# Kernel tuning notes

Measured on AMD Instinct MI355X. Metric: run time of the kernel, lower is better.

## Reference

```python
import jax, jax.numpy as jnp
import numpy as np

B, N, C, HEADS = 4, 8192, 512, 8


def setup_inputs() -> dict:
    key = jax.random.key(0)
    k1, k2, k3, k4, k5 = jax.random.split(key, 5)
    s = 1.0 / np.sqrt(C)
    return {
        "x": jax.random.normal(k1, (B, N, C), dtype=jnp.float32),
        "w_qkv": jax.random.normal(k2, (3 * C, C), dtype=jnp.float32) * s,
        "b_qkv": jax.random.normal(k3, (3 * C,), dtype=jnp.float32) * 0.01,
        "w_fc": jax.random.normal(k4, (C, C), dtype=jnp.float32) * s,
        "b_fc": jax.random.normal(k5, (C,), dtype=jnp.float32) * 0.01,
        "heads": HEADS,
    }


def reference(x, w_qkv, b_qkv, w_fc, b_fc, heads):
    b, n, c = x.shape
    d = c // heads
    scale = d ** (-0.5)
    # torch Linear: y = x @ W.T + b
    qkv = (x @ w_qkv.T + b_qkv).reshape(b, n, 3, heads, d)
    q, k, v = qkv[:, :, 0], qkv[:, :, 1], qkv[:, :, 2]  # [b,n,h,d]
    # NOTE: source does NOT move heads to dim 1, so attention is over the
    # heads axis: dots is [b, n, h, h].
    dots = jnp.einsum("bnhd,bngd->bnhg", q, k) * scale
    dots = jnp.clip(dots, -50.0, 50.0)
    attn = jax.nn.softmax(dots, axis=-1)
    out = jnp.einsum("bnhg,bngd->bnhd", attn, v)  # [b,n,h,d]
    # transpose(1,2).reshape(B,N,C) exactly as in torch (scrambles n/h)
    out = out.transpose(0, 2, 1, 3).reshape(b, n, c)
    return out @ w_fc.T + b_fc
```

## Files before the change

### kernel.cpp

```cpp
#include <hip/hip_runtime.h>
#include <hip/hip_bf16.h>
#include <stdint.h>


typedef __bf16 bf16x8 __attribute__((ext_vector_type(8)));
typedef float f32x4 __attribute__((ext_vector_type(4)));

__device__ __forceinline__ unsigned short f2bf(float f) {
  unsigned u = __float_as_uint(f);
  u += 0x7fffu + ((u >> 16) & 1u);
  return (unsigned short)(u >> 16);
}
__device__ __forceinline__ unsigned pk2(float a, float b) {
  return (unsigned)f2bf(a) | ((unsigned)f2bf(b) << 16);
}
__device__ __forceinline__ void unpk2(unsigned u, float& a, float& b) {
  a = __uint_as_float(u << 16);
  b = __uint_as_float(u & 0xffff0000u);
}
__device__ __forceinline__ void gload_lds16(const void* g, void* l) {
  __builtin_amdgcn_global_load_lds((const __attribute__((address_space(1))) void*)g,
                                   (__attribute__((address_space(3))) void*)l,
                                   16, 0, 0);
}

__global__ __launch_bounds__(256) void cvt_f32_to_bf16(const float* __restrict__ in,
                                                       __hip_bfloat16* __restrict__ out,
                                                       int n8) {
  int i = blockIdx.x * 256 + threadIdx.x;
  if (i >= n8) return;
  const float4* p = (const float4*)in;
  float4 a = p[i * 2];
  float4 b = p[i * 2 + 1];
  uint4 o;
  o.x = pk2(a.x, a.y);
  o.y = pk2(a.z, a.w);
  o.z = pk2(b.x, b.y);
  o.w = pk2(b.z, b.w);
  ((uint4*)out)[i] = o;
}


#define STG(S, BUF)                                                                       \
  do {                                                                                    \
    int _k0 = (S) * 32;                                                                   \
    gload_lds16(Ag + (size_t)(bm0 + srowA0) * KDIM + _k0 + skofA0,                        \
                lds + (BUF) * 24576 + dstA0);                                             \
    gload_lds16(Ag + (size_t)(bm0 + srowA1) * KDIM + _k0 + skofA1,                        \
                lds + (BUF) * 24576 + dstA1);                                             \
    gload_lds16(Bg + (size_t)(bn0 + srowB) * KDIM + _k0 + skofB,                          \
                lds + (BUF) * 24576 + 16384 + dstB);                                      \
  } while (0)

template <bool OUT_BF16, int KDIM>
__global__ __launch_bounds__(512, 4) void gemm3b(const __hip_bfloat16* __restrict__ Ag,
                                                 const __hip_bfloat16* __restrict__ Bg,
                                                 const float* __restrict__ bias,
                                                 void* __restrict__ C,
                                                 int M, int N, int NT) {
  __shared__ __align__(16) char lds[73728];

  const int tid = threadIdx.x;
  const int wv = tid >> 6;
  const int ln = tid & 63;
  const int lrow = ln & 15;
  const int kg = ln >> 4;
  const int wm = wv >> 1;
  const int wn = wv & 1;

  int nwg = gridDim.x;
  int cpx = nwg >> 3;
  int bs = (blockIdx.x & 7) * cpx + (blockIdx.x >> 3);
  const int bm0 = (bs / NT) * 256;
  const int bn0 = (bs % NT) * 128;

  const int pbase = (lrow >> 1) * 128 + ((((lrow & 1) << 2) | kg) ^ ((lrow >> 1) & 7)) * 16;

  int srowA0, skofA0, dstA0, srowA1, skofA1, dstA1, srowB, skofB, dstB;
  {
    int L0 = wv * 1024 + ln * 16;
    int rp0 = L0 >> 7, T0 = ((L0 >> 4) & 7) ^ (rp0 & 7);
    srowA0 = rp0 * 2 + (T0 >> 2);
    skofA0 = (T0 & 3) * 8;
    dstA0 = wv * 1024;
    int L1 = 8192 + L0;
    int rp1 = L1 >> 7, T1 = ((L1 >> 4) & 7) ^ (rp1 & 7);
    srowA1 = rp1 * 2 + (T1 >> 2);
    skofA1 = (T1 & 3) * 8;
    dstA1 = 8192 + wv * 1024;
    srowB = srowA0;
    skofB = skofA0;
    dstB = wv * 1024;
  }

  f32x4 acc[4][4] = {};

  constexpr int NKT = KDIM >> 5;

  STG(0, 0);
  STG(1, 1);

#pragma unroll
  for (int s = 0; s < NKT; ++s) {
    if (s == NKT - 1) {
      asm volatile("s_waitcnt vmcnt(0)" ::: "memory");
    } else {
      asm volatile("s_waitcnt vmcnt(3)" ::: "memory");
    }
    __builtin_amdgcn_s_barrier();
    __builtin_amdgcn_sched_barrier(0);
    if (s + 2 < NKT) STG(s + 2, (s + 2) % 3);
    {
      const char* _ab = lds + (s % 3) * 24576 + wm * 4096 + pbase;
      const char* _bb = lds + (s % 3) * 24576 + 16384 + wn * 4096 + pbase;
      bf16x8 a0 = *(const bf16x8*)(_ab);
      bf16x8 a1 = *(const bf16x8*)(_ab + 1024);
      bf16x8 a2 = *(const bf16x8*)(_ab + 2048);
      bf16x8 a3 = *(const bf16x8*)(_ab + 3072);
      bf16x8 b0 = *(const bf16x8*)(_bb);
      bf16x8 b1 = *(const bf16x8*)(_bb + 1024);
      bf16x8 b2 = *(const bf16x8*)(_bb + 2048);
      bf16x8 b3 = *(const bf16x8*)(_bb + 3072);
      asm volatile("s_waitcnt lgkmcnt(0)" ::: "memory");
      __builtin_amdgcn_sched_barrier(0);
      __builtin_amdgcn_s_setprio(1);
      acc[0][0] = __builtin_amdgcn_mfma_f32_16x16x32_bf16(a0, b0, acc[0][0], 0, 0, 0);
      acc[0][1] = __builtin_amdgcn_mfma_f32_16x16x32_bf16(a0, b1, acc[0][1], 0, 0, 0);
      acc[0][2] = __builtin_amdgcn_mfma_f32_16x16x32_bf16(a0, b2, acc[0][2], 0, 0, 0);
      acc[0][3] = __builtin_amdgcn_mfma_f32_16x16x32_bf16(a0, b3, acc[0][3], 0, 0, 0);
      acc[1][0] = __builtin_amdgcn_mfma_f32_16x16x32_bf16(a1, b0, acc[1][0], 0, 0, 0);
      acc[1][1] = __builtin_amdgcn_mfma_f32_16x16x32_bf16(a1, b1, acc[1][1], 0, 0, 0);
      acc[1][2] = __builtin_amdgcn_mfma_f32_16x16x32_bf16(a1, b2, acc[1][2], 0, 0, 0);
      acc[1][3] = __builtin_amdgcn_mfma_f32_16x16x32_bf16(a1, b3, acc[1][3], 0, 0, 0);
      acc[2][0] = __builtin_amdgcn_mfma_f32_16x16x32_bf16(a2, b0, acc[2][0], 0, 0, 0);
      acc[2][1] = __builtin_amdgcn_mfma_f32_16x16x32_bf16(a2, b1, acc[2][1], 0, 0, 0);
      acc[2][2] = __builtin_amdgcn_mfma_f32_16x16x32_bf16(a2, b2, acc[2][2], 0, 0, 0);
      acc[2][3] = __builtin_amdgcn_mfma_f32_16x16x32_bf16(a2, b3, acc[2][3], 0, 0, 0);
      acc[3][0] = __builtin_amdgcn_mfma_f32_16x16x32_bf16(a3, b0, acc[3][0], 0, 0, 0);
      acc[3][1] = __builtin_amdgcn_mfma_f32_16x16x32_bf16(a3, b1, acc[3][1], 0, 0, 0);
      acc[3][2] = __builtin_amdgcn_mfma_f32_16x16x32_bf16(a3, b2, acc[3][2], 0, 0, 0);
      acc[3][3] = __builtin_amdgcn_mfma_f32_16x16x32_bf16(a3, b3, acc[3][3], 0, 0, 0);
      __builtin_amdgcn_s_setprio(0);
    }
  }
  __syncthreads();

  if (OUT_BF16) {
    unsigned short* tile = (unsigned short*)lds;
#pragma unroll
    for (int fi = 0; fi < 4; ++fi) {
#pragma unroll
      for (int cj = 0; cj < 4; ++cj) {
        int col = wn * 64 + cj * 16 + lrow;
        float bv = bias[bn0 + col];
#pragma unroll
        for (int r = 0; r < 4; ++r) {
          int row = wm * 64 + fi * 16 + kg * 4 + r;
          int sc = (((col >> 3) ^ (row & 7)) << 3) | (col & 7);
          tile[row * 128 + sc] = f2bf(acc[fi][cj][r] + bv);
        }
      }
    }
    __syncthreads();
#pragma unroll
    for (int it = 0; it < 8; ++it) {
      int id = it * 512 + tid;
      int row = id >> 4;
      int c = id & 15;
      uint4 v = *(const uint4*)(lds + row * 256 + ((c ^ (row & 7)) << 4));
      *(uint4*)((unsigned short*)C + (size_t)(bm0 + row) * N + bn0 + c * 8) = v;
    }
  } else {
    float* tilef = (float*)lds;
#pragma unroll
    for (int pass = 0; pass < 2; ++pass) {
      if ((wm >> 1) == pass) {
#pragma unroll
        for (int fi = 0; fi < 4; ++fi) {
#pragma unroll
          for (int cj = 0; cj < 4; ++cj) {
            int col = wn * 64 + cj * 16 + lrow;
            float bv = bias[bn0 + col];
#pragma unroll
            for (int r = 0; r < 4; ++r) {
              int row = (wm & 1) * 64 + fi * 16 + kg * 4 + r;
              int sc = (((col >> 2) ^ (row & 7)) << 2) | (col & 3);
              tilef[row * 128 + sc] = acc[fi][cj][r] + bv;
            }
          }
        }
      }
      __syncthreads();
#pragma unroll
      for (int it = 0; it < 8; ++it) {
        int id = it * 512 + tid;
        int row = id >> 5;
        int c = id & 31;
        uint4 v = *(const uint4*)(lds + row * 512 + ((c ^ (row & 7)) << 4));
        *(uint4*)((float*)C + (size_t)(bm0 + pass * 128 + row) * N + bn0 + c * 4) = v;
      }
      __syncthreads();
    }
  }
}

__global__ __launch_bounds__(256) void attn_tok(const __hip_bfloat16* __restrict__ qkv,
                                                __hip_bfloat16* __restrict__ outp,
                                                int ntok, int npb) {
  const int wv = threadIdx.x >> 6;
  const int ln = threadIdx.x & 63;
  const int t = blockIdx.x * 4 + wv;
  if (t >= ntok) return;
  const int m = ln & 7;

  const __hip_bfloat16* row = qkv + (size_t)t * 1536;
  uint4 qr = *(const uint4*)(row + ln * 8);
  uint4 kr = *(const uint4*)(row + 512 + ln * 8);
  uint4 vr = *(const uint4*)(row + 1024 + ln * 8);

  float qf[8];
  unpk2(qr.x, qf[0], qf[1]);
  unpk2(qr.y, qf[2], qf[3]);
  unpk2(qr.z, qf[4], qf[5]);
  unpk2(qr.w, qf[6], qf[7]);
  unsigned kw[4] = {kr.x, kr.y, kr.z, kr.w};
  unsigned vw[4] = {vr.x, vr.y, vr.z, vr.w};

  float dt[8];
#pragma unroll
  for (int g = 0; g < 8; ++g) {
    int src = g * 8 + m;
    float s = 0.f;
#pragma unroll
    for (int j4 = 0; j4 < 4; ++j4) {
      unsigned kk = __shfl(kw[j4], src, 64);
      float a, b;
      unpk2(kk, a, b);
      s += qf[j4 * 2] * a + qf[j4 * 2 + 1] * b;
    }
    s += __shfl_xor(s, 1, 64);
    s += __shfl_xor(s, 2, 64);
    s += __shfl_xor(s, 4, 64);
    dt[g] = s;
  }

  float mx = -1e30f;
#pragma unroll
  for (int g = 0; g < 8; ++g) {
    dt[g] = fminf(fmaxf(dt[g] * 0.125f, -50.f), 50.f);
    mx = fmaxf(mx, dt[g]);
  }
  float p[8], ssum = 0.f;
#pragma unroll
  for (int g = 0; g < 8; ++g) {
    p[g] = __expf(dt[g] - mx);
    ssum += p[g];
  }
  float inv = 1.f / ssum;

  float o[8] = {0, 0, 0, 0, 0, 0, 0, 0};
#pragma unroll
  for (int g = 0; g < 8; ++g) {
    int src = g * 8 + m;
    float ag = p[g] * inv;
#pragma unroll
    for (int j4 = 0; j4 < 4; ++j4) {
      unsigned vv = __shfl(vw[j4], src, 64);
      float a, b;
      unpk2(vv, a, b);
      o[j4 * 2] += ag * a;
      o[j4 * 2 + 1] += ag * b;
    }
  }

  const int h = ln >> 3;
  const int b = t / npb, n = t % npb;
  size_t dst = (size_t)b * npb * 512 + (size_t)(h * (npb >> 3) + (n >> 3)) * 512 +
               (size_t)((n & 7) * 64 + m * 8);
  uint4 ov;
  ov.x = pk2(o[0], o[1]);
  ov.y = pk2(o[2], o[3]);
  ov.z = pk2(o[4], o[5]);
  ov.w = pk2(o[6], o[7]);
  *(uint4*)(outp + dst) = ov;
}

extern "C" void kernel_launch(void* const* d_in, const int* in_sizes, int n_in,
                              void* d_out, int out_size, void* d_ws, size_t ws_size,
                              hipStream_t stream) {
  const float* x = (const float*)d_in[0];
  const float* w_qkv = (const float*)d_in[1];
  const float* b_qkv = (const float*)d_in[2];
  const float* w_fc = (const float*)d_in[3];
  const float* b_fc = (const float*)d_in[4];
  float* out = (float*)d_out;

  const int M = 32768;
  const int Cc = 512, N3 = 1536;

  __hip_bfloat16* xb = (__hip_bfloat16*)d_ws;
  __hip_bfloat16* wqkvb = xb + (size_t)M * Cc;
  __hip_bfloat16* wfcb = wqkvb + (size_t)N3 * Cc;
  __hip_bfloat16* qkvb = wfcb + (size_t)Cc * Cc;
  __hip_bfloat16* attb = qkvb + (size_t)M * N3;

  cvt_f32_to_bf16<<<(M * Cc / 8) / 256, 256, 0, stream>>>(x, xb, M * Cc / 8);
  cvt_f32_to_bf16<<<(N3 * Cc / 8) / 256, 256, 0, stream>>>(w_qkv, wqkvb, N3 * Cc / 8);
  cvt_f32_to_bf16<<<(Cc * Cc / 8) / 256, 256, 0, stream>>>(w_fc, wfcb, Cc * Cc / 8);

  gemm3b<true, 512><<<(M / 256) * (N3 / 128), 512, 0, stream>>>(xb, wqkvb, b_qkv, qkvb, M, N3,
                                                                N3 / 128);
  attn_tok<<<M / 4, 256, 0, stream>>>(qkvb, attb, M, 8192);
  gemm3b<false, 512><<<(M / 256) * (Cc / 128), 512, 0, stream>>>(attb, wfcb, b_fc, out, M, Cc,
                                                                 Cc / 128);
}
```

Measured before the change: 147.4 us.

## Use 4-wave GEMM blocks with 128x64 per-wave tiles

Restructures the GEMM kernel from 8 waves of 64x64 subtiles to 4 waves of 128x64 subtiles over the same 256x128 block tile. Each wave now issues 6 global-to-LDS loads per stage and keeps 32 accumulators, which raises the MFMA-to-LDS-read ratio and halves barrier participants. The cost is higher register pressure and fewer waves to hide latency, and the launch bounds change to 256 threads with 2 blocks per unit.

```diff
diff --git a/kernel.cpp b/kernel.cpp
--- a/kernel.cpp
+++ b/kernel.cpp
@@ -44,16 +44,18 @@
 #define STG(S, BUF)                                                                       \
   do {                                                                                    \
     int _k0 = (S) * 32;                                                                   \
-    gload_lds16(Ag + (size_t)(bm0 + srowA0) * KDIM + _k0 + skofA0,                        \
-                lds + (BUF) * 24576 + dstA0);                                             \
-    gload_lds16(Ag + (size_t)(bm0 + srowA1) * KDIM + _k0 + skofA1,                        \
-                lds + (BUF) * 24576 + dstA1);                                             \
-    gload_lds16(Bg + (size_t)(bn0 + srowB) * KDIM + _k0 + skofB,                          \
-                lds + (BUF) * 24576 + 16384 + dstB);                                      \
+    _Pragma("unroll") for (int _j = 0; _j < 4; ++_j) {                                    \
+      gload_lds16(Ag + (size_t)(bm0 + srowA[_j]) * KDIM + _k0 + skofA[_j],                \
+                  lds + (BUF) * 24576 + _j * 4096 + wv * 1024);                           \
+    }                                                                                     \
+    _Pragma("unroll") for (int _j = 0; _j < 2; ++_j) {                                    \
+      gload_lds16(Bg + (size_t)(bn0 + srowB[_j]) * KDIM + _k0 + skofB[_j],                \
+                  lds + (BUF) * 24576 + 16384 + _j * 4096 + wv * 1024);                   \
+    }                                                                                     \
   } while (0)
 
 template <bool OUT_BF16, int KDIM>
-__global__ __launch_bounds__(512, 4) void gemm3b(const __hip_bfloat16* __restrict__ Ag,
+__global__ __launch_bounds__(256, 2) void gemm4w(const __hip_bfloat16* __restrict__ Ag,
                                                  const __hip_bfloat16* __restrict__ Bg,
                                                  const float* __restrict__ bias,
                                                  void* __restrict__ C,
@@ -76,24 +78,20 @@
 
   const int pbase = (lrow >> 1) * 128 + ((((lrow & 1) << 2) | kg) ^ ((lrow >> 1) & 7)) * 16;
 
-  int srowA0, skofA0, dstA0, srowA1, skofA1, dstA1, srowB, skofB, dstB;
-  {
-    int L0 = wv * 1024 + ln * 16;
-    int rp0 = L0 >> 7, T0 = ((L0 >> 4) & 7) ^ (rp0 & 7);
-    srowA0 = rp0 * 2 + (T0 >> 2);
-    skofA0 = (T0 & 3) * 8;
-    dstA0 = wv * 1024;
-    int L1 = 8192 + L0;
-    int rp1 = L1 >> 7, T1 = ((L1 >> 4) & 7) ^ (rp1 & 7);
-    srowA1 = rp1 * 2 + (T1 >> 2);
-    skofA1 = (T1 & 3) * 8;
-    dstA1 = 8192 + wv * 1024;
-    srowB = srowA0;
-    skofB = skofA0;
-    dstB = wv * 1024;
-  }
-
-  f32x4 acc[4][4] = {};
+  int srowA[4], skofA[4], srowB[2], skofB[2];
+#pragma unroll
+  for (int j = 0; j < 4; ++j) {
+    int L = j * 4096 + wv * 1024 + ln * 16;
+    int rp = L >> 7, T = ((L >> 4) & 7) ^ (rp & 7);
+    srowA[j] = rp * 2 + (T >> 2);
+    skofA[j] = (T & 3) * 8;
+    if (j < 2) {
+      srowB[j] = srowA[j];
+      skofB[j] = skofA[j];
+    }
+  }
+
+  f32x4 acc[8][4] = {};
 
   constexpr int NKT = KDIM >> 5;
 
@@ -105,41 +103,29 @@
     if (s == NKT - 1) {
       asm volatile("s_waitcnt vmcnt(0)" ::: "memory");
     } else {
-      asm volatile("s_waitcnt vmcnt(3)" ::: "memory");
+      asm volatile("s_waitcnt vmcnt(6)" ::: "memory");
     }
     __builtin_amdgcn_s_barrier();
     __builtin_amdgcn_sched_barrier(0);
     if (s + 2 < NKT) STG(s + 2, (s + 2) % 3);
     {
-      const char* _ab = lds + (s % 3) * 24576 + wm * 4096 + pbase;
+      const char* _ab = lds + (s % 3) * 24576 + wm * 8192 + pbase;
       const char* _bb = lds + (s % 3) * 24576 + 16384 + wn * 4096 + pbase;
-      bf16x8 a0 = *(const bf16x8*)(_ab);
-      bf16x8 a1 = *(const bf16x8*)(_ab + 1024);
-      bf16x8 a2 = *(const bf16x8*)(_ab + 2048);
-      bf16x8 a3 = *(const bf16x8*)(_ab + 3072);
-      bf16x8 b0 = *(const bf16x8*)(_bb);
-      bf16x8 b1 = *(const bf16x8*)(_bb + 1024);
-      bf16x8 b2 = *(const bf16x8*)(_bb + 2048);
-      bf16x8 b3 = *(const bf16x8*)(_bb + 3072);
+      bf16x8 af[8];
+      bf16x8 bf[4];
+#pragma unroll
+      for (int fi = 0; fi < 8; ++fi) af[fi] = *(const bf16x8*)(_ab + fi * 1024);
+#pragma unroll
+      for (int cj = 0; cj < 4; ++cj) bf[cj] = *(const bf16x8*)(_bb + cj * 1024);
       asm volatile("s_waitcnt lgkmcnt(0)" ::: "memory");
       __builtin_amdgcn_sched_barrier(0);
       __builtin_amdgcn_s_setprio(1);
-      acc[0][0] = __builtin_amdgcn_mfma_f32_16x16x32_bf16(a0, b0, acc[0][0], 0, 0, 0);
-      acc[0][1] = __builtin_amdgcn_mfma_f32_16x16x32_bf16(a0, b1, acc[0][1], 0, 0, 0);
-      acc[0][2] = __builtin_amdgcn_mfma_f32_16x16x32_bf16(a0, b2, acc[0][2], 0, 0, 0);
-      acc[0][3] = __builtin_amdgcn_mfma_f32_16x16x32_bf16(a0, b3, acc[0][3], 0, 0, 0);
-      acc[1][0] = __builtin_amdgcn_mfma_f32_16x16x32_bf16(a1, b0, acc[1][0], 0, 0, 0);
-      acc[1][1] = __builtin_amdgcn_mfma_f32_16x16x32_bf16(a1, b1, acc[1][1], 0, 0, 0);
-      acc[1][2] = __builtin_amdgcn_mfma_f32_16x16x32_bf16(a1, b2, acc[1][2], 0, 0, 0);
-      acc[1][3] = __builtin_amdgcn_mfma_f32_16x16x32_bf16(a1, b3, acc[1][3], 0, 0, 0);
-      acc[2][0] = __builtin_amdgcn_mfma_f32_16x16x32_bf16(a2, b0, acc[2][0], 0, 0, 0);
-      acc[2][1] = __builtin_amdgcn_mfma_f32_16x16x32_bf16(a2, b1, acc[2][1], 0, 0, 0);
-      acc[2][2] = __builtin_amdgcn_mfma_f32_16x16x32_bf16(a2, b2, acc[2][2], 0, 0, 0);
-      acc[2][3] = __builtin_amdgcn_mfma_f32_16x16x32_bf16(a2, b3, acc[2][3], 0, 0, 0);
-      acc[3][0] = __builtin_amdgcn_mfma_f32_16x16x32_bf16(a3, b0, acc[3][0], 0, 0, 0);
-      acc[3][1] = __builtin_amdgcn_mfma_f32_16x16x32_bf16(a3, b1, acc[3][1], 0, 0, 0);
-      acc[3][2] = __builtin_amdgcn_mfma_f32_16x16x32_bf16(a3, b2, acc[3][2], 0, 0, 0);
-      acc[3][3] = __builtin_amdgcn_mfma_f32_16x16x32_bf16(a3, b3, acc[3][3], 0, 0, 0);
+#pragma unroll
+      for (int fi = 0; fi < 8; ++fi)
+#pragma unroll
+        for (int cj = 0; cj < 4; ++cj)
+          acc[fi][cj] =
+              __builtin_amdgcn_mfma_f32_16x16x32_bf16(af[fi], bf[cj], acc[fi][cj], 0, 0, 0);
       __builtin_amdgcn_s_setprio(0);
     }
   }
@@ -148,14 +134,14 @@
   if (OUT_BF16) {
     unsigned short* tile = (unsigned short*)lds;
 #pragma unroll
-    for (int fi = 0; fi < 4; ++fi) {
+    for (int fi = 0; fi < 8; ++fi) {
 #pragma unroll
       for (int cj = 0; cj < 4; ++cj) {
         int col = wn * 64 + cj * 16 + lrow;
         float bv = bias[bn0 + col];
 #pragma unroll
         for (int r = 0; r < 4; ++r) {
-          int row = wm * 64 + fi * 16 + kg * 4 + r;
+          int row = wm * 128 + fi * 16 + kg * 4 + r;
           int sc = (((col >> 3) ^ (row & 7)) << 3) | (col & 7);
           tile[row * 128 + sc] = f2bf(acc[fi][cj][r] + bv);
         }
@@ -163,8 +149,8 @@
     }
     __syncthreads();
 #pragma unroll
-    for (int it = 0; it < 8; ++it) {
-      int id = it * 512 + tid;
+    for (int it = 0; it < 16; ++it) {
+      int id = it * 256 + tid;
       int row = id >> 4;
       int c = id & 15;
       uint4 v = *(const uint4*)(lds + row * 256 + ((c ^ (row & 7)) << 4));
@@ -174,16 +160,16 @@
     float* tilef = (float*)lds;
 #pragma unroll
     for (int pass = 0; pass < 2; ++pass) {
-      if ((wm >> 1) == pass) {
-#pragma unroll
-        for (int fi = 0; fi < 4; ++fi) {
+      if (wm == pass) {
+#pragma unroll
+        for (int fi = 0; fi < 8; ++fi) {
 #pragma unroll
           for (int cj = 0; cj < 4; ++cj) {
             int col = wn * 64 + cj * 16 + lrow;
             float bv = bias[bn0 + col];
 #pragma unroll
             for (int r = 0; r < 4; ++r) {
-              int row = (wm & 1) * 64 + fi * 16 + kg * 4 + r;
+              int row = fi * 16 + kg * 4 + r;
               int sc = (((col >> 2) ^ (row & 7)) << 2) | (col & 3);
               tilef[row * 128 + sc] = acc[fi][cj][r] + bv;
             }
@@ -192,8 +178,8 @@
       }
       __syncthreads();
 #pragma unroll
-      for (int it = 0; it < 8; ++it) {
-        int id = it * 512 + tid;
+      for (int it = 0; it < 16; ++it) {
+        int id = it * 256 + tid;
         int row = id >> 5;
         int c = id & 31;
         uint4 v = *(const uint4*)(lds + row * 512 + ((c ^ (row & 7)) << 4));
@@ -308,9 +294,9 @@
   cvt_f32_to_bf16<<<(N3 * Cc / 8) / 256, 256, 0, stream>>>(w_qkv, wqkvb, N3 * Cc / 8);
   cvt_f32_to_bf16<<<(Cc * Cc / 8) / 256, 256, 0, stream>>>(w_fc, wfcb, Cc * Cc / 8);
 
-  gemm3b<true, 512><<<(M / 256) * (N3 / 128), 512, 0, stream>>>(xb, wqkvb, b_qkv, qkvb, M, N3,
+  gemm4w<true, 512><<<(M / 256) * (N3 / 128), 256, 0, stream>>>(xb, wqkvb, b_qkv, qkvb, M, N3,
                                                                 N3 / 128);
   attn_tok<<<M / 4, 256, 0, stream>>>(qkvb, attb, M, 8192);
-  gemm3b<false, 512><<<(M / 256) * (Cc / 128), 512, 0, stream>>>(attb, wfcb, b_fc, out, M, Cc,
+  gemm4w<false, 512><<<(M / 256) * (Cc / 128), 256, 0, stream>>>(attb, wfcb, b_fc, out, M, Cc,
                                                                  Cc / 128);
 }
```

New measurement: 154.5 us. +4.9%, slower.

## Switch GEMM to 32x32x16 MFMA tiles and fuse the three conversion kernels

Applied to the files above, without the earlier changes.

The GEMM inner loop moves from sixteen 16x16x32 MFMAs per k-step to eight 32x32x16 MFMAs on four 32x32 accumulators. LDS fragment addressing and the epilogue row/column mapping change to match the 32x32 output layout. The aim is fewer MFMA issues and fewer LDS reads per unit of work. The three f32-to-bf16 conversion launches are also merged into a single kernel that picks its source by index range, which removes two launch overheads. The risk is that the new lane-to-element mapping, which relies on the swizzle, gives wrong results if it does not line up with the staging layout.

```diff
diff --git a/kernel.cpp b/kernel.cpp
--- a/kernel.cpp
+++ b/kernel.cpp
@@ -5,6 +5,7 @@
 
 typedef __bf16 bf16x8 __attribute__((ext_vector_type(8)));
 typedef float f32x4 __attribute__((ext_vector_type(4)));
+typedef float f32x16 __attribute__((ext_vector_type(16)));
 
 __device__ __forceinline__ unsigned short f2bf(float f) {
   unsigned u = __float_as_uint(f);
@@ -24,20 +25,34 @@
                                    16, 0, 0);
 }
 
-__global__ __launch_bounds__(256) void cvt_f32_to_bf16(const float* __restrict__ in,
-                                                       __hip_bfloat16* __restrict__ out,
-                                                       int n8) {
+__global__ __launch_bounds__(256) void cvt_all(const float* __restrict__ x,
+                                               const float* __restrict__ wq,
+                                               const float* __restrict__ wf,
+                                               unsigned short* __restrict__ xb,
+                                               unsigned short* __restrict__ wqb,
+                                               unsigned short* __restrict__ wfb) {
+  const int n0 = 2097152;
+  const int n1 = 98304;
   int i = blockIdx.x * 256 + threadIdx.x;
-  if (i >= n8) return;
+  const float* in;
+  unsigned short* ob;
+  int j;
+  if (i < n0) {
+    in = x; ob = xb; j = i;
+  } else if (i < n0 + n1) {
+    in = wq; ob = wqb; j = i - n0;
+  } else {
+    in = wf; ob = wfb; j = i - n0 - n1;
+  }
   const float4* p = (const float4*)in;
-  float4 a = p[i * 2];
-  float4 b = p[i * 2 + 1];
+  float4 a = p[j * 2];
+  float4 b = p[j * 2 + 1];
   uint4 o;
   o.x = pk2(a.x, a.y);
   o.y = pk2(a.z, a.w);
   o.z = pk2(b.x, b.y);
   o.w = pk2(b.z, b.w);
-  ((uint4*)out)[i] = o;
+  ((uint4*)ob)[j] = o;
 }
 
 
@@ -53,7 +68,7 @@
   } while (0)
 
 template <bool OUT_BF16, int KDIM>
-__global__ __launch_bounds__(512, 4) void gemm3b(const __hip_bfloat16* __restrict__ Ag,
+__global__ __launch_bounds__(512, 4) void gemm32(const __hip_bfloat16* __restrict__ Ag,
                                                  const __hip_bfloat16* __restrict__ Bg,
                                                  const float* __restrict__ bias,
                                                  void* __restrict__ C,
@@ -63,8 +78,8 @@
   const int tid = threadIdx.x;
   const int wv = tid >> 6;
   const int ln = tid & 63;
-  const int lrow = ln & 15;
-  const int kg = ln >> 4;
+  const int lr32 = ln & 31;
+  const int kh = ln >> 5;
   const int wm = wv >> 1;
   const int wn = wv & 1;
 
@@ -74,7 +89,12 @@
   const int bm0 = (bs / NT) * 256;
   const int bn0 = (bs % NT) * 128;
 
-  const int pbase = (lrow >> 1) * 128 + ((((lrow & 1) << 2) | kg) ^ ((lrow >> 1) & 7)) * 16;
+  const int pA = (wm * 32 + (lr32 >> 1)) * 128;
+  const int pB = (wn * 32 + (lr32 >> 1)) * 128;
+  const int x7 = (lr32 >> 1) & 7;
+  const int e4 = (lr32 & 1) << 2;
+  const int sl0 = ((e4 | kh) ^ x7) * 16;
+  const int sl1 = ((e4 | (2 + kh)) ^ x7) * 16;
 
   int srowA0, skofA0, dstA0, srowA1, skofA1, dstA1, srowB, skofB, dstB;
   {
@@ -93,7 +113,7 @@
     dstB = wv * 1024;
   }
 
-  f32x4 acc[4][4] = {};
+  f32x16 acc00 = {}, acc01 = {}, acc10 = {}, acc11 = {};
 
   constexpr int NKT = KDIM >> 5;
 
@@ -111,35 +131,27 @@
     __builtin_amdgcn_sched_barrier(0);
     if (s + 2 < NKT) STG(s + 2, (s + 2) % 3);
     {
-      const char* _ab = lds + (s % 3) * 24576 + wm * 4096 + pbase;
-      const char* _bb = lds + (s % 3) * 24576 + 16384 + wn * 4096 + pbase;
-      bf16x8 a0 = *(const bf16x8*)(_ab);
-      bf16x8 a1 = *(const bf16x8*)(_ab + 1024);
-      bf16x8 a2 = *(const bf16x8*)(_ab + 2048);
-      bf16x8 a3 = *(const bf16x8*)(_ab + 3072);
-      bf16x8 b0 = *(const bf16x8*)(_bb);
-      bf16x8 b1 = *(const bf16x8*)(_bb + 1024);
-      bf16x8 b2 = *(const bf16x8*)(_bb + 2048);
-      bf16x8 b3 = *(const bf16x8*)(_bb + 3072);
+      const char* rgA = lds + (s % 3) * 24576;
+      const char* rgB = rgA + 16384;
+      bf16x8 a00 = *(const bf16x8*)(rgA + pA + sl0);
+      bf16x8 a01 = *(const bf16x8*)(rgA + pA + sl1);
+      bf16x8 a10 = *(const bf16x8*)(rgA + pA + 2048 + sl0);
+      bf16x8 a11 = *(const bf16x8*)(rgA + pA + 2048 + sl1);
+      bf16x8 b00 = *(const bf16x8*)(rgB + pB + sl0);
+      bf16x8 b01 = *(const bf16x8*)(rgB + pB + sl1);
+      bf16x8 b10 = *(const bf16x8*)(rgB + pB + 2048 + sl0);
+      bf16x8 b11 = *(const bf16x8*)(rgB + pB + 2048 + sl1);
       asm volatile("s_waitcnt lgkmcnt(0)" ::: "memory");
       __builtin_amdgcn_sched_barrier(0);
       __builtin_amdgcn_s_setprio(1);
-      acc[0][0] = __builtin_amdgcn_mfma_f32_16x16x32_bf16(a0, b0, acc[0][0], 0, 0, 0);
-      acc[0][1] = __builtin_amdgcn_mfma_f32_16x16x32_bf16(a0, b1, acc[0][1], 0, 0, 0);
-      acc[0][2] = __builtin_amdgcn_mfma_f32_16x16x32_bf16(a0, b2, acc[0][2], 0, 0, 0);
-      acc[0][3] = __builtin_amdgcn_mfma_f32_16x16x32_bf16(a0, b3, acc[0][3], 0, 0, 0);
-      acc[1][0] = __builtin_amdgcn_mfma_f32_16x16x32_bf16(a1, b0, acc[1][0], 0, 0, 0);
-      acc[1][1] = __builtin_amdgcn_mfma_f32_16x16x32_bf16(a1, b1, acc[1][1], 0, 0, 0);
-      acc[1][2] = __builtin_amdgcn_mfma_f32_16x16x32_bf16(a1, b2, acc[1][2], 0, 0, 0);
-      acc[1][3] = __builtin_amdgcn_mfma_f32_16x16x32_bf16(a1, b3, acc[1][3], 0, 0, 0);
-      acc[2][0] = __builtin_amdgcn_mfma_f32_16x16x32_bf16(a2, b0, acc[2][0], 0, 0, 0);
-      acc[2][1] = __builtin_amdgcn_mfma_f32_16x16x32_bf16(a2, b1, acc[2][1], 0, 0, 0);
-      acc[2][2] = __builtin_amdgcn_mfma_f32_16x16x32_bf16(a2, b2, acc[2][2], 0, 0, 0);
-      acc[2][3] = __builtin_amdgcn_mfma_f32_16x16x32_bf16(a2, b3, acc[2][3], 0, 0, 0);
-      acc[3][0] = __builtin_amdgcn_mfma_f32_16x16x32_bf16(a3, b0, acc[3][0], 0, 0, 0);
-      acc[3][1] = __builtin_amdgcn_mfma_f32_16x16x32_bf16(a3, b1, acc[3][1], 0, 0, 0);
-      acc[3][2] = __builtin_amdgcn_mfma_f32_16x16x32_bf16(a3, b2, acc[3][2], 0, 0, 0);
-      acc[3][3] = __builtin_amdgcn_mfma_f32_16x16x32_bf16(a3, b3, acc[3][3], 0, 0, 0);
+      acc00 = __builtin_amdgcn_mfma_f32_32x32x16_bf16(a00, b00, acc00, 0, 0, 0);
+      acc00 = __builtin_amdgcn_mfma_f32_32x32x16_bf16(a01, b01, acc00, 0, 0, 0);
+      acc01 = __builtin_amdgcn_mfma_f32_32x32x16_bf16(a00, b10, acc01, 0, 0, 0);
+      acc01 = __builtin_amdgcn_mfma_f32_32x32x16_bf16(a01, b11, acc01, 0, 0, 0);
+      acc10 = __builtin_amdgcn_mfma_f32_32x32x16_bf16(a10, b00, acc10, 0, 0, 0);
+      acc10 = __builtin_amdgcn_mfma_f32_32x32x16_bf16(a11, b01, acc10, 0, 0, 0);
+      acc11 = __builtin_amdgcn_mfma_f32_32x32x16_bf16(a10, b10, acc11, 0, 0, 0);
+      acc11 = __builtin_amdgcn_mfma_f32_32x32x16_bf16(a11, b11, acc11, 0, 0, 0);
       __builtin_amdgcn_s_setprio(0);
     }
   }
@@ -148,16 +160,17 @@
   if (OUT_BF16) {
     unsigned short* tile = (unsigned short*)lds;
 #pragma unroll
-    for (int fi = 0; fi < 4; ++fi) {
-#pragma unroll
-      for (int cj = 0; cj < 4; ++cj) {
-        int col = wn * 64 + cj * 16 + lrow;
+    for (int rb = 0; rb < 2; ++rb) {
+#pragma unroll
+      for (int cb = 0; cb < 2; ++cb) {
+        const f32x16& A = rb == 0 ? (cb == 0 ? acc00 : acc01) : (cb == 0 ? acc10 : acc11);
+        int col = wn * 64 + cb * 32 + lr32;
         float bv = bias[bn0 + col];
 #pragma unroll
-        for (int r = 0; r < 4; ++r) {
-          int row = wm * 64 + fi * 16 + kg * 4 + r;
+        for (int reg = 0; reg < 16; ++reg) {
+          int row = wm * 64 + rb * 32 + (reg & 3) + 8 * (reg >> 2) + 4 * kh;
           int sc = (((col >> 3) ^ (row & 7)) << 3) | (col & 7);
-          tile[row * 128 + sc] = f2bf(acc[fi][cj][r] + bv);
+          tile[row * 128 + sc] = f2bf(A[reg] + bv);
         }
       }
     }
@@ -176,16 +189,17 @@
     for (int pass = 0; pass < 2; ++pass) {
       if ((wm >> 1) == pass) {
 #pragma unroll
-        for (int fi = 0; fi < 4; ++fi) {
-#pragma unroll
-          for (int cj = 0; cj < 4; ++cj) {
-            int col = wn * 64 + cj * 16 + lrow;
+        for (int rb = 0; rb < 2; ++rb) {
+#pragma unroll
+          for (int cb = 0; cb < 2; ++cb) {
+            const f32x16& A = rb == 0 ? (cb == 0 ? acc00 : acc01) : (cb == 0 ? acc10 : acc11);
+            int col = wn * 64 + cb * 32 + lr32;
             float bv = bias[bn0 + col];
 #pragma unroll
-            for (int r = 0; r < 4; ++r) {
-              int row = (wm & 1) * 64 + fi * 16 + kg * 4 + r;
+            for (int reg = 0; reg < 16; ++reg) {
+              int row = (wm & 1) * 64 + rb * 32 + (reg & 3) + 8 * (reg >> 2) + 4 * kh;
               int sc = (((col >> 2) ^ (row & 7)) << 2) | (col & 3);
-              tilef[row * 128 + sc] = acc[fi][cj][r] + bv;
+              tilef[row * 128 + sc] = A[reg] + bv;
             }
           }
         }
@@ -304,13 +318,12 @@
   __hip_bfloat16* qkvb = wfcb + (size_t)Cc * Cc;
   __hip_bfloat16* attb = qkvb + (size_t)M * N3;
 
-  cvt_f32_to_bf16<<<(M * Cc / 8) / 256, 256, 0, stream>>>(x, xb, M * Cc / 8);
-  cvt_f32_to_bf16<<<(N3 * Cc / 8) / 256, 256, 0, stream>>>(w_qkv, wqkvb, N3 * Cc / 8);
-  cvt_f32_to_bf16<<<(Cc * Cc / 8) / 256, 256, 0, stream>>>(w_fc, wfcb, Cc * Cc / 8);
-
-  gemm3b<true, 512><<<(M / 256) * (N3 / 128), 512, 0, stream>>>(xb, wqkvb, b_qkv, qkvb, M, N3,
+  cvt_all<<<8704, 256, 0, stream>>>(x, w_qkv, w_fc, (unsigned short*)xb,
+                                    (unsigned short*)wqkvb, (unsigned short*)wfcb);
+
+  gemm32<true, 512><<<(M / 256) * (N3 / 128), 512, 0, stream>>>(xb, wqkvb, b_qkv, qkvb, M, N3,
                                                                 N3 / 128);
   attn_tok<<<M / 4, 256, 0, stream>>>(qkvb, attb, M, 8192);
-  gemm3b<false, 512><<<(M / 256) * (Cc / 128), 512, 0, stream>>>(attb, wfcb, b_fc, out, M, Cc,
+  gemm32<false, 512><<<(M / 256) * (Cc / 128), 512, 0, stream>>>(attb, wfcb, b_fc, out, M, Cc,
                                                                  Cc / 128);
 }
```

Measured after the change: 150.9 us. +2.4%, slower.

## Prefetch next K-step LDS fragments during MFMAs and merge conversion kernels

Applied to the files above, without the earlier changes.

The GEMM main loop now uses register double-buffering. The A and B fragments for the next K-step are read from LDS while the current step's MFMAs issue, which removes the lgkmcnt(0) stall before each MFMA block. The wait per step changes from vmcnt(3) to vmcnt(0), so each step waits for the most recent global-to-LDS prefetch and global-load overlap may shrink. The three fp32-to-bf16 conversion launches are merged into one kernel that picks its source by thread index, saving launch overhead.

```diff
diff --git a/kernel.cpp b/kernel.cpp
--- a/kernel.cpp
+++ b/kernel.cpp
@@ -24,20 +24,34 @@
                                    16, 0, 0);
 }
 
-__global__ __launch_bounds__(256) void cvt_f32_to_bf16(const float* __restrict__ in,
-                                                       __hip_bfloat16* __restrict__ out,
-                                                       int n8) {
+__global__ __launch_bounds__(256) void cvt_all(const float* __restrict__ x,
+                                               const float* __restrict__ wq,
+                                               const float* __restrict__ wf,
+                                               unsigned short* __restrict__ xb,
+                                               unsigned short* __restrict__ wqb,
+                                               unsigned short* __restrict__ wfb) {
+  const int n0 = 2097152;
+  const int n1 = 98304;
   int i = blockIdx.x * 256 + threadIdx.x;
-  if (i >= n8) return;
+  const float* in;
+  unsigned short* ob;
+  int j;
+  if (i < n0) {
+    in = x; ob = xb; j = i;
+  } else if (i < n0 + n1) {
+    in = wq; ob = wqb; j = i - n0;
+  } else {
+    in = wf; ob = wfb; j = i - n0 - n1;
+  }
   const float4* p = (const float4*)in;
-  float4 a = p[i * 2];
-  float4 b = p[i * 2 + 1];
+  float4 a = p[j * 2];
+  float4 b = p[j * 2 + 1];
   uint4 o;
   o.x = pk2(a.x, a.y);
   o.y = pk2(a.z, a.w);
   o.z = pk2(b.x, b.y);
   o.w = pk2(b.z, b.w);
-  ((uint4*)out)[i] = o;
+  ((uint4*)ob)[j] = o;
 }
 
 
@@ -52,12 +66,38 @@
                 lds + (BUF) * 24576 + 16384 + dstB);                                      \
   } while (0)
 
+#define STEP(S, BC, BN)                                                                   \
+  do {                                                                                    \
+    const int s_ = (S);                                                                   \
+    asm volatile("s_waitcnt vmcnt(0)" ::: "memory");             \
+    __builtin_amdgcn_s_barrier();                                \
+    __builtin_amdgcn_sched_barrier(0);                                                    \
+    if (s_ + 2 < NKT) STG(s_ + 2, (s_ + 2) % 3);                                          \
+    const char* nab = lds + ((s_ + 1) % 3) * 24576 + wm * 4096 + pbase;                   \
+    const char* nbb = lds + ((s_ + 1) % 3) * 24576 + 16384 + wn * 4096 + pbase;           \
+    if (s_ + 1 < NKT) {                                                                   \
+      BN[0] = *(const bf16x8*)(nbb);                                                      \
+      BN[1] = *(const bf16x8*)(nbb + 1024);                                               \
+      BN[2] = *(const bf16x8*)(nbb + 2048);                                               \
+      BN[3] = *(const bf16x8*)(nbb + 3072);                                               \
+    }                                                                                     \
+    __builtin_amdgcn_s_setprio(1);                                                        \
+    _Pragma("unroll") for (int _i = 0; _i < 4; ++_i) {                                    \
+      acc[_i][0] = __builtin_amdgcn_mfma_f32_16x16x32_bf16(af[_i], BC[0], acc[_i][0], 0, 0, 0); \
+      acc[_i][1] = __builtin_amdgcn_mfma_f32_16x16x32_bf16(af[_i], BC[1], acc[_i][1], 0, 0, 0); \
+      acc[_i][2] = __builtin_amdgcn_mfma_f32_16x16x32_bf16(af[_i], BC[2], acc[_i][2], 0, 0, 0); \
+      acc[_i][3] = __builtin_amdgcn_mfma_f32_16x16x32_bf16(af[_i], BC[3], acc[_i][3], 0, 0, 0); \
+      if (s_ + 1 < NKT) af[_i] = *(const bf16x8*)(nab + _i * 1024);                       \
+    }                                                                                     \
+    __builtin_amdgcn_s_setprio(0);                                                        \
+  } while (0)
+
 template <bool OUT_BF16, int KDIM>
-__global__ __launch_bounds__(512, 4) void gemm3b(const __hip_bfloat16* __restrict__ Ag,
-                                                 const __hip_bfloat16* __restrict__ Bg,
-                                                 const float* __restrict__ bias,
-                                                 void* __restrict__ C,
-                                                 int M, int N, int NT) {
+__global__ __launch_bounds__(512, 4) void gemmp(const __hip_bfloat16* __restrict__ Ag,
+                                                const __hip_bfloat16* __restrict__ Bg,
+                                                const float* __restrict__ bias,
+                                                void* __restrict__ C,
+                                                int M, int N, int NT) {
   __shared__ __align__(16) char lds[73728];
 
   const int tid = threadIdx.x;
@@ -94,54 +134,28 @@
   }
 
   f32x4 acc[4][4] = {};
+  bf16x8 af[4], bs0[4], bs1[4];
 
   constexpr int NKT = KDIM >> 5;
 
   STG(0, 0);
   STG(1, 1);
-
-#pragma unroll
-  for (int s = 0; s < NKT; ++s) {
-    if (s == NKT - 1) {
-      asm volatile("s_waitcnt vmcnt(0)" ::: "memory");
-    } else {
-      asm volatile("s_waitcnt vmcnt(3)" ::: "memory");
-    }
-    __builtin_amdgcn_s_barrier();
-    __builtin_amdgcn_sched_barrier(0);
-    if (s + 2 < NKT) STG(s + 2, (s + 2) % 3);
-    {
-      const char* _ab = lds + (s % 3) * 24576 + wm * 4096 + pbase;
-      const char* _bb = lds + (s % 3) * 24576 + 16384 + wn * 4096 + pbase;
-      bf16x8 a0 = *(const bf16x8*)(_ab);
-      bf16x8 a1 = *(const bf16x8*)(_ab + 1024);
-      bf16x8 a2 = *(const bf16x8*)(_ab + 2048);
-      bf16x8 a3 = *(const bf16x8*)(_ab + 3072);
-      bf16x8 b0 = *(const bf16x8*)(_bb);
-      bf16x8 b1 = *(const bf16x8*)(_bb + 1024);
-      bf16x8 b2 = *(const bf16x8*)(_bb + 2048);
-      bf16x8 b3 = *(const bf16x8*)(_bb + 3072);
-      asm volatile("s_waitcnt lgkmcnt(0)" ::: "memory");
-      __builtin_amdgcn_sched_barrier(0);
-      __builtin_amdgcn_s_setprio(1);
-      acc[0][0] = __builtin_amdgcn_mfma_f32_16x16x32_bf16(a0, b0, acc[0][0], 0, 0, 0);
-      acc[0][1] = __builtin_amdgcn_mfma_f32_16x16x32_bf16(a0, b1, acc[0][1], 0, 0, 0);
-      acc[0][2] = __builtin_amdgcn_mfma_f32_16x16x32_bf16(a0, b2, acc[0][2], 0, 0, 0);
-      acc[0][3] = __builtin_amdgcn_mfma_f32_16x16x32_bf16(a0, b3, acc[0][3], 0, 0, 0);
-      acc[1][0] = __builtin_amdgcn_mfma_f32_16x16x32_bf16(a1, b0, acc[1][0], 0, 0, 0);
-      acc[1][1] = __builtin_amdgcn_mfma_f32_16x16x32_bf16(a1, b1, acc[1][1], 0, 0, 0);
-      acc[1][2] = __builtin_amdgcn_mfma_f32_16x16x32_bf16(a1, b2, acc[1][2], 0, 0, 0);
-      acc[1][3] = __builtin_amdgcn_mfma_f32_16x16x32_bf16(a1, b3, acc[1][3], 0, 0, 0);
-      acc[2][0] = __builtin_amdgcn_mfma_f32_16x16x32_bf16(a2, b0, acc[2][0], 0, 0, 0);
-      acc[2][1] = __builtin_amdgcn_mfma_f32_16x16x32_bf16(a2, b1, acc[2][1], 0, 0, 0);
-      acc[2][2] = __builtin_amdgcn_mfma_f32_16x16x32_bf16(a2, b2, acc[2][2], 0, 0, 0);
-      acc[2][3] = __builtin_amdgcn_mfma_f32_16x16x32_bf16(a2, b3, acc[2][3], 0, 0, 0);
-      acc[3][0] = __builtin_amdgcn_mfma_f32_16x16x32_bf16(a3, b0, acc[3][0], 0, 0, 0);
-      acc[3][1] = __builtin_amdgcn_mfma_f32_16x16x32_bf16(a3, b1, acc[3][1], 0, 0, 0);
-      acc[3][2] = __builtin_amdgcn_mfma_f32_16x16x32_bf16(a3, b2, acc[3][2], 0, 0, 0);
-      acc[3][3] = __builtin_amdgcn_mfma_f32_16x16x32_bf16(a3, b3, acc[3][3], 0, 0, 0);
-      __builtin_amdgcn_s_setprio(0);
-    }
+  asm volatile("s_waitcnt vmcnt(3)" ::: "memory");
+  __builtin_amdgcn_s_barrier();
+  __builtin_amdgcn_sched_barrier(0);
+  {
+    const char* ab0 = lds + wm * 4096 + pbase;
+    const char* bb0 = lds + 16384 + wn * 4096 + pbase;
+#pragma unroll
+    for (int i = 0; i < 4; ++i) af[i] = *(const bf16x8*)(ab0 + i * 1024);
+#pragma unroll
+    for (int j = 0; j < 4; ++j) bs0[j] = *(const bf16x8*)(bb0 + j * 1024);
+  }
+
+#pragma unroll
+  for (int sp = 0; sp < NKT / 2; ++sp) {
+    STEP(2 * sp, bs0, bs1);
+    STEP(2 * sp + 1, bs1, bs0);
   }
   __syncthreads();
 
@@ -304,13 +318,12 @@
   __hip_bfloat16* qkvb = wfcb + (size_t)Cc * Cc;
   __hip_bfloat16* attb = qkvb + (size_t)M * N3;
 
-  cvt_f32_to_bf16<<<(M * Cc / 8) / 256, 256, 0, stream>>>(x, xb, M * Cc / 8);
-  cvt_f32_to_bf16<<<(N3 * Cc / 8) / 256, 256, 0, stream>>>(w_qkv, wqkvb, N3 * Cc / 8);
-  cvt_f32_to_bf16<<<(Cc * Cc / 8) / 256, 256, 0, stream>>>(w_fc, wfcb, Cc * Cc / 8);
-
-  gemm3b<true, 512><<<(M / 256) * (N3 / 128), 512, 0, stream>>>(xb, wqkvb, b_qkv, qkvb, M, N3,
-                                                                N3 / 128);
+  cvt_all<<<8704, 256, 0, stream>>>(x, w_qkv, w_fc, (unsigned short*)xb,
+                                    (unsigned short*)wqkvb, (unsigned short*)wfcb);
+
+  gemmp<true, 512><<<(M / 256) * (N3 / 128), 512, 0, stream>>>(xb, wqkvb, b_qkv, qkvb, M, N3,
+                                                               N3 / 128);
   attn_tok<<<M / 4, 256, 0, stream>>>(qkvb, attb, M, 8192);
-  gemm3b<false, 512><<<(M / 256) * (Cc / 128), 512, 0, stream>>>(attb, wfcb, b_fc, out, M, Cc,
-                                                                 Cc / 128);
-}
+  gemmp<false, 512><<<(M / 256) * (Cc / 128), 512, 0, stream>>>(attb, wfcb, b_fc, out, M, Cc,
+                                                                Cc / 128);
+}
```

Result: no change. 146.3 us, median of 2 (-0.7%).
